# Performance work log

Measured on AMD Instinct MI355X. Metric: run time of the kernel, lower is better.

The kernel has to match this reference:

```python
import jax, jax.numpy as jnp
import numpy as np

NEG_SLOPE = 0.2
EPS = 1e-16  # PyG softmax denominator epsilon


def _gatv2_layer(x, src, dst, n_nodes, W_l, W_r, att, bias):
    """Single-head GATv2Conv (PyG defaults, self loops already in src/dst).
    x: [N, F_in]; src/dst: [E]; W_l/W_r: [F_in, F_out]; att: [F_out]; bias: [F_out].
    """
    x_l = x @ W_l                       # source transform [N, F_out]
    x_r = x @ W_r                       # target transform [N, F_out]
    # per-edge attention logit: a^T LeakyReLU(x_l[j] + x_r[i])
    e = jax.nn.leaky_relu(x_l[src] + x_r[dst], NEG_SLOPE) @ att  # [E]
    # softmax over incoming edges of each destination node
    e_max = jax.ops.segment_max(e, dst, num_segments=n_nodes)    # [N]
    ex = jnp.exp(e - e_max[dst])                                  # [E]
    denom = jax.ops.segment_sum(ex, dst, num_segments=n_nodes)   # [N]
    alpha = ex / (denom[dst] + EPS)                               # [E]
    out = jax.ops.segment_sum(alpha[:, None] * x_l[src], dst, num_segments=n_nodes)
    return out + bias


def setup_inputs() -> dict:
    key = jax.random.key(0)
    N, E = 50000, 800000
    IN, HID, OUT = 128, 64, 64
    ks = jax.random.split(key, 12)
    x = jax.random.normal(ks[0], (N, IN), dtype=jnp.float32)
    edge_index = jax.random.randint(ks[1], (2, E), 0, N, dtype=jnp.int64)
    s1 = float(1.0 / np.sqrt(IN))
    s2 = float(1.0 / np.sqrt(HID))
    return {
        "x": x,
        "edge_index": edge_index,
        "W1_l": jax.random.uniform(ks[2], (IN, HID), jnp.float32, -s1, s1),
        "W1_r": jax.random.uniform(ks[3], (IN, HID), jnp.float32, -s1, s1),
        "att1": jax.random.uniform(ks[4], (HID,), jnp.float32, -s2, s2),
        "b1": jnp.zeros((HID,), jnp.float32),
        "W2_l": jax.random.uniform(ks[5], (HID, OUT), jnp.float32, -s2, s2),
        "W2_r": jax.random.uniform(ks[6], (HID, OUT), jnp.float32, -s2, s2),
        "att2": jax.random.uniform(ks[7], (OUT,), jnp.float32, -s2, s2),
        "b2": jnp.zeros((OUT,), jnp.float32),
    }


def reference(x, edge_index, W1_l, W1_r, att1, b1, W2_l, W2_r, att2, b2):
    n = x.shape[0]
    loop = jnp.arange(n, dtype=edge_index.dtype)
    src = jnp.concatenate([edge_index[0], loop])  # add self loops (PyG default)
    dst = jnp.concatenate([edge_index[1], loop])
    h = _gatv2_layer(x, src, dst, n, W1_l, W1_r, att1, b1)
    h = jax.nn.relu(h)
    out = _gatv2_layer(h, src, dst, n, W2_l, W2_r, att2, b2)
    return out
```

## Files before the change

kernel.cpp:

```cpp
#include <hip/hip_runtime.h>
#include <math.h>

#define NEG_SLOPE 0.2f
#define EPSV 1e-16f
#define NEG_HUGE -1e30f
#define CAP 64
#define GH 1024

typedef short short8 __attribute__((ext_vector_type(8)));
typedef float f32x4 __attribute__((ext_vector_type(4)));
typedef unsigned short u16;


__global__ __launch_bounds__(256) void k_wpack(
        const float* __restrict__ W1l, const float* __restrict__ W1r,
        const float* __restrict__ W2l, const float* __restrict__ W2r,
        u16* __restrict__ w1hi, u16* __restrict__ w1lo,
        u16* __restrict__ w2hi, u16* __restrict__ w2lo,
        int* __restrict__ cnt, u16* __restrict__ csrc, int N, int NP) {
    const int idx = blockIdx.x * 256 + threadIdx.x;
    const int G = gridDim.x * 256;
    const int CN = 8 * NP;
    for (int i = idx; i < CN; i += G) {
        const int cls = i / NP;
        const int r = i - cls * NP;
        const int d = r * 8 + cls;
        cnt[i] = (d < N) ? 1 : 0;
    }
    for (int d = idx; d < N; d += G) csrc[(size_t)d * CAP] = (u16)d;
    const int T1 = 128 * 128, T2 = 64 * 128;
    if (idx >= T1 + T2) return;
    u16 *dhi, *dlo; const float *Wl, *Wr; int li;
    if (idx < T1) { dhi = w1hi; dlo = w1lo; Wl = W1l; Wr = W1r; li = idx; }
    else          { dhi = w2hi; dlo = w2lo; Wl = W2l; Wr = W2r; li = idx - T1; }
    const int j = li & 7, l = (li >> 3) & 63, t = (li >> 9) & 7, c = li >> 12;
    const int k = c * 32 + (l >> 4) * 8 + j;
    const int n = t * 16 + (l & 15);
    const float v = (n < 64) ? Wl[k * 64 + n] : Wr[k * 64 + (n - 64)];
    const unsigned u = __float_as_uint(v);
    dhi[li] = (u16)(u >> 16);
    const float hif = __uint_as_float(u & 0xffff0000u);
    dlo[li] = (u16)(__float_as_uint(v - hif) >> 16);
}

__device__ __forceinline__ void split8(const float* fs, short8& ahi, short8& alo) {
#pragma unroll
    for (int j = 0; j < 8; ++j) {
        const unsigned u = __float_as_uint(fs[j]);
        ahi[j] = (short)(u >> 16);
        const float hif = __uint_as_float(u & 0xffff0000u);
        alo[j] = (short)(__float_as_uint(fs[j] - hif) >> 16);
    }
}

template <int K>
__device__ __forceinline__ void gemm_mfma_tile(const float* __restrict__ X,
                                               const u16* __restrict__ whi,
                                               const u16* __restrict__ wlo,
                                               float* __restrict__ xl,
                                               float* __restrict__ xr,
                                               int N, int tile) {
    const int lane = threadIdx.x & 63;
    const int w = threadIdx.x >> 6;
    const int rowbase = tile * 64 + w * 16;
    const int m = lane & 15, q = lane >> 4;
    int ar = rowbase + m; if (ar > N - 1) ar = N - 1;
    const float* arow = X + (size_t)ar * K + q * 8;
    f32x4 acc[8];
#pragma unroll
    for (int t = 0; t < 8; ++t) acc[t] = (f32x4){0.f, 0.f, 0.f, 0.f};
#pragma unroll
    for (int c = 0; c < K / 32; ++c) {
        const f32x4 f0 = __builtin_nontemporal_load((const f32x4*)(arow + c * 32));
        const f32x4 f1 = __builtin_nontemporal_load((const f32x4*)(arow + c * 32 + 4));
        const float fs[8] = {f0[0], f0[1], f0[2], f0[3], f1[0], f1[1], f1[2], f1[3]};
        short8 ahi, alo;
        split8(fs, ahi, alo);
        const u16* bp = whi + ((size_t)(c * 8) * 64 + lane) * 8;
        const u16* bq = wlo + ((size_t)(c * 8) * 64 + lane) * 8;
#pragma unroll
        for (int t = 0; t < 8; ++t) {
            const short8 bhi = *(const short8*)(bp + t * 64 * 8);
            const short8 blo = *(const short8*)(bq + t * 64 * 8);
            acc[t] = __builtin_amdgcn_mfma_f32_16x16x32_bf16(bhi, ahi, acc[t], 0, 0, 0);
            acc[t] = __builtin_amdgcn_mfma_f32_16x16x32_bf16(blo, ahi, acc[t], 0, 0, 0);
            acc[t] = __builtin_amdgcn_mfma_f32_16x16x32_bf16(bhi, alo, acc[t], 0, 0, 0);
        }
    }
    const int row = rowbase + m;
    if (row < N) {
#pragma unroll
        for (int t = 0; t < 8; ++t) {
            const int colb = t * 16 + q * 4;
            float* dstp = (t < 4) ? (xl + (size_t)row * 64 + colb)
                                  : (xr + (size_t)row * 64 + (colb - 64));
            __builtin_nontemporal_store(acc[t], (f32x4*)dstp);
        }
    }
}

template <int K>
__global__ __launch_bounds__(256) void k_hist_gemm(const int* __restrict__ ei, int E,
                                                   int* __restrict__ cnt,
                                                   u16* __restrict__ csrc,
                                                   const float* __restrict__ X,
                                                   const u16* __restrict__ whi,
                                                   const u16* __restrict__ wlo,
                                                   float* __restrict__ xl,
                                                   float* __restrict__ xr,
                                                   int N, int NP) {
    if ((int)blockIdx.x < GH) {
        const int cls = blockIdx.x & 7;
        const int stripe = blockIdx.x >> 3;
        const int NS = GH >> 3;
        const int tid = threadIdx.x;
        const int* srcp = ei;
        const int* dstp = ei + E;
        int* cntc = cnt + cls * NP;
        if ((E & 7) == 0) {
            for (int base = stripe * 2048; base < E; base += NS * 2048) {
                const int e8 = base + tid * 8;
                if (e8 < E) {
                    const int4 da = *(const int4*)(dstp + e8);
                    const int4 db = *(const int4*)(dstp + e8 + 4);
                    const int4 sa = *(const int4*)(srcp + e8);
                    const int4 sb = *(const int4*)(srcp + e8 + 4);
                    const int d[8] = {da.x, da.y, da.z, da.w, db.x, db.y, db.z, db.w};
                    const int s[8] = {sa.x, sa.y, sa.z, sa.w, sb.x, sb.y, sb.z, sb.w};
                    bool m[8]; int sl[8];
#pragma unroll
                    for (int j = 0; j < 8; ++j) {
                        m[j] = (d[j] & 7) == cls;
                        if (m[j]) sl[j] = atomicAdd(&cntc[d[j] >> 3], 1);
                    }
#pragma unroll
                    for (int j = 0; j < 8; ++j) {
                        if (m[j]) csrc[(size_t)d[j] * CAP + sl[j]] = (u16)s[j];
                    }
                }
            }
        } else {
            for (int base = stripe * 256; base < E; base += NS * 256) {
                const int e = base + tid;
                if (e < E) {
                    const int dd = dstp[e];
                    if ((dd & 7) == cls) {
                        const int ss = srcp[e];
                        const int slot = atomicAdd(&cntc[dd >> 3], 1);
                        csrc[(size_t)dd * CAP + slot] = (u16)ss;
                    }
                }
            }
        }
    } else {
        gemm_mfma_tile<K>(X, whi, wlo, xl, xr, N, blockIdx.x - GH);
    }
}

template <int K>
__global__ __launch_bounds__(256) void k_gemm(const float* __restrict__ X,
                                              const u16* __restrict__ whi,
                                              const u16* __restrict__ wlo,
                                              float* __restrict__ xl,
                                              float* __restrict__ xr, int N) {
    gemm_mfma_tile<K>(X, whi, wlo, xl, xr, N, blockIdx.x);
}

__global__ __launch_bounds__(256) void k_attn(const float* __restrict__ xl,
                                              const float* xr,
                                              const float* __restrict__ att,
                                              const int* __restrict__ cnt,
                                              const u16* __restrict__ csrc,
                                              const float* __restrict__ bias,
                                              float* out, int N, int NP, int relu) {
    const int lane = threadIdx.x & 63;
    const int g = lane >> 4;
    const int i = lane & 15;
    const int dst = blockIdx.x * 4 + (threadIdx.x >> 6);
    if (dst >= N) return;
    const float4 xrv = *(const float4*)(xr + (size_t)dst * 64 + i * 4);
    const float4 aw  = *(const float4*)(att + i * 4);
    const int deg = cnt[(dst & 7) * NP + (dst >> 3)];
    const int sidx = (int)csrc[(size_t)dst * CAP + ((lane < deg) ? lane : 0)];
    float l = 0.0f;
    float4 acc = {0.0f, 0.0f, 0.0f, 0.0f};
    for (int t = 0; t < deg; t += 16) {
        const int s0 = t + g, s1 = t + 4 + g, s2 = t + 8 + g, s3 = t + 12 + g;
        const bool v0 = s0 < deg, v1 = s1 < deg, v2 = s2 < deg, v3 = s3 < deg;
        const int src0 = __shfl(sidx, s0, 64);
        const int src1 = __shfl(sidx, s1, 64);
        const int src2 = __shfl(sidx, s2, 64);
        const int src3 = __shfl(sidx, s3, 64);
        const float4 va = *(const float4*)(xl + (size_t)src0 * 64 + i * 4);
        const float4 vb = *(const float4*)(xl + (size_t)src1 * 64 + i * 4);
        const float4 vc = *(const float4*)(xl + (size_t)src2 * 64 + i * 4);
        const float4 vd = *(const float4*)(xl + (size_t)src3 * 64 + i * 4);
        float t0, p0, p1, p2, p3;
        t0 = va.x + xrv.x; t0 = fmaxf(t0, NEG_SLOPE * t0); p0 = aw.x * t0;
        t0 = va.y + xrv.y; t0 = fmaxf(t0, NEG_SLOPE * t0); p0 = fmaf(aw.y, t0, p0);
        t0 = va.z + xrv.z; t0 = fmaxf(t0, NEG_SLOPE * t0); p0 = fmaf(aw.z, t0, p0);
        t0 = va.w + xrv.w; t0 = fmaxf(t0, NEG_SLOPE * t0); p0 = fmaf(aw.w, t0, p0);
        t0 = vb.x + xrv.x; t0 = fmaxf(t0, NEG_SLOPE * t0); p1 = aw.x * t0;
        t0 = vb.y + xrv.y; t0 = fmaxf(t0, NEG_SLOPE * t0); p1 = fmaf(aw.y, t0, p1);
        t0 = vb.z + xrv.z; t0 = fmaxf(t0, NEG_SLOPE * t0); p1 = fmaf(aw.z, t0, p1);
        t0 = vb.w + xrv.w; t0 = fmaxf(t0, NEG_SLOPE * t0); p1 = fmaf(aw.w, t0, p1);
        t0 = vc.x + xrv.x; t0 = fmaxf(t0, NEG_SLOPE * t0); p2 = aw.x * t0;
        t0 = vc.y + xrv.y; t0 = fmaxf(t0, NEG_SLOPE * t0); p2 = fmaf(aw.y, t0, p2);
        t0 = vc.z + xrv.z; t0 = fmaxf(t0, NEG_SLOPE * t0); p2 = fmaf(aw.z, t0, p2);
        t0 = vc.w + xrv.w; t0 = fmaxf(t0, NEG_SLOPE * t0); p2 = fmaf(aw.w, t0, p2);
        t0 = vd.x + xrv.x; t0 = fmaxf(t0, NEG_SLOPE * t0); p3 = aw.x * t0;
        t0 = vd.y + xrv.y; t0 = fmaxf(t0, NEG_SLOPE * t0); p3 = fmaf(aw.y, t0, p3);
        t0 = vd.z + xrv.z; t0 = fmaxf(t0, NEG_SLOPE * t0); p3 = fmaf(aw.z, t0, p3);
        t0 = vd.w + xrv.w; t0 = fmaxf(t0, NEG_SLOPE * t0); p3 = fmaf(aw.w, t0, p3);
        p0 += __shfl_xor(p0, 1, 64); p1 += __shfl_xor(p1, 1, 64);
        p2 += __shfl_xor(p2, 1, 64); p3 += __shfl_xor(p3, 1, 64);
        p0 += __shfl_xor(p0, 2, 64); p1 += __shfl_xor(p1, 2, 64);
        p2 += __shfl_xor(p2, 2, 64); p3 += __shfl_xor(p3, 2, 64);
        p0 += __shfl_xor(p0, 4, 64); p1 += __shfl_xor(p1, 4, 64);
        p2 += __shfl_xor(p2, 4, 64); p3 += __shfl_xor(p3, 4, 64);
        p0 += __shfl_xor(p0, 8, 64); p1 += __shfl_xor(p1, 8, 64);
        p2 += __shfl_xor(p2, 8, 64); p3 += __shfl_xor(p3, 8, 64);
        const float d0 = __expf(v0 ? p0 : NEG_HUGE);
        const float d1 = __expf(v1 ? p1 : NEG_HUGE);
        const float d2 = __expf(v2 ? p2 : NEG_HUGE);
        const float d3 = __expf(v3 ? p3 : NEG_HUGE);
        l += (d0 + d1) + (d2 + d3);
        acc.x = fmaf(d0, va.x, fmaf(d1, vb.x, fmaf(d2, vc.x, fmaf(d3, vd.x, acc.x))));
        acc.y = fmaf(d0, va.y, fmaf(d1, vb.y, fmaf(d2, vc.y, fmaf(d3, vd.y, acc.y))));
        acc.z = fmaf(d0, va.z, fmaf(d1, vb.z, fmaf(d2, vc.z, fmaf(d3, vd.z, acc.z))));
        acc.w = fmaf(d0, va.w, fmaf(d1, vb.w, fmaf(d2, vc.w, fmaf(d3, vd.w, acc.w))));
    }
#pragma unroll
    for (int o = 16; o <= 32; o <<= 1) {
        l     += __shfl_xor(l, o, 64);
        acc.x += __shfl_xor(acc.x, o, 64);
        acc.y += __shfl_xor(acc.y, o, 64);
        acc.z += __shfl_xor(acc.z, o, 64);
        acc.w += __shfl_xor(acc.w, o, 64);
    }
    if (g == 0) {
        const float4 bv = *(const float4*)(bias + i * 4);
        const float inv = 1.0f / (l + EPSV);
        float4 r;
        r.x = fmaf(acc.x, inv, bv.x);
        r.y = fmaf(acc.y, inv, bv.y);
        r.z = fmaf(acc.z, inv, bv.z);
        r.w = fmaf(acc.w, inv, bv.w);
        if (relu) {
            r.x = fmaxf(r.x, 0.0f); r.y = fmaxf(r.y, 0.0f);
            r.z = fmaxf(r.z, 0.0f); r.w = fmaxf(r.w, 0.0f);
        }
        *(float4*)(out + (size_t)dst * 64 + i * 4) = r;
    }
}


extern "C" void kernel_launch(void* const* d_in, const int* in_sizes, int n_in,
                              void* d_out, int out_size, void* d_ws, size_t ws_size,
                              hipStream_t stream) {
    const float* x    = (const float*)d_in[0];
    const int*   ei   = (const int*)d_in[1];
    const float* W1l  = (const float*)d_in[2];
    const float* W1r  = (const float*)d_in[3];
    const float* att1 = (const float*)d_in[4];
    const float* b1   = (const float*)d_in[5];
    const float* W2l  = (const float*)d_in[6];
    const float* W2r  = (const float*)d_in[7];
    const float* att2 = (const float*)d_in[8];
    const float* b2   = (const float*)d_in[9];

    const int N  = in_sizes[0] / 128;
    const int E  = in_sizes[1] / 2;
    const int NP = (((N + 7) >> 3) + 31) & ~31;

    int* wsi   = (int*)d_ws;
    int* cnt   = wsi;
    u16* csrc  = (u16*)(cnt + 8 * NP);
    u16* w1hi  = csrc + (size_t)N * CAP;
    u16* w1lo  = w1hi + 16384;
    u16* w2hi  = w1lo + 16384;
    u16* w2lo  = w2hi + 8192;
    float* buf1 = (float*)(w2lo + 8192);
    float* buf2 = buf1 + (size_t)N * 64;
    float* fout = (float*)d_out;

    const dim3 b256(256);
    const int gGemm = (N + 63) / 64;
    const int gAttn = (N + 3) / 4;

    k_wpack<<<(128 * 128 + 64 * 128 + 255) / 256, b256, 0, stream>>>(
        W1l, W1r, W2l, W2r, w1hi, w1lo, w2hi, w2lo, cnt, csrc, N, NP);

    k_hist_gemm<128><<<GH + gGemm, b256, 0, stream>>>(ei, E, cnt, csrc,
                                                      x, w1hi, w1lo, fout, buf1, N, NP);
    k_attn<<<gAttn, b256, 0, stream>>>(fout, buf1, att1, cnt, csrc, b1, buf2, N, NP, 1);

    k_gemm<64><<<gGemm, b256, 0, stream>>>(buf2, w2hi, w2lo, buf1, fout, N);
    k_attn<<<gAttn, b256, 0, stream>>>(buf1, fout, att2, cnt, csrc, b2, fout, N, NP, 0);
}
```

Measured before the change: 228.1 us.

## Split fused histogram/GEMM kernel into separate build and GEMM launches

Undoes the fusion of the CSR bucket build and the layer-1 MFMA GEMM, turning them back into two kernel launches. The build kernel now uses 2048 blocks that each process 4 edges per thread instead of 8. The GEMM tile switches from nontemporal loads and stores to plain vector loads and stores, and the k_wpack grid is fixed at 256 blocks. Running the two phases separately loses their concurrent overlap and adds a launch, in exchange for simpler scheduling and more parallelism in the atomic build.

```diff
diff --git a/kernel.cpp b/kernel.cpp
--- a/kernel.cpp
+++ b/kernel.cpp
@@ -5,7 +5,7 @@
 #define EPSV 1e-16f
 #define NEG_HUGE -1e30f
 #define CAP 64
-#define GH 1024
+#define GB 2048
 
 typedef short short8 __attribute__((ext_vector_type(8)));
 typedef float f32x4 __attribute__((ext_vector_type(4)));
@@ -71,9 +71,9 @@
     for (int t = 0; t < 8; ++t) acc[t] = (f32x4){0.f, 0.f, 0.f, 0.f};
 #pragma unroll
     for (int c = 0; c < K / 32; ++c) {
-        const f32x4 f0 = __builtin_nontemporal_load((const f32x4*)(arow + c * 32));
-        const f32x4 f1 = __builtin_nontemporal_load((const f32x4*)(arow + c * 32 + 4));
-        const float fs[8] = {f0[0], f0[1], f0[2], f0[3], f1[0], f1[1], f1[2], f1[3]};
+        const float4 f0 = *(const float4*)(arow + c * 32);
+        const float4 f1 = *(const float4*)(arow + c * 32 + 4);
+        const float fs[8] = {f0.x, f0.y, f0.z, f0.w, f1.x, f1.y, f1.z, f1.w};
         short8 ahi, alo;
         split8(fs, ahi, alo);
         const u16* bp = whi + ((size_t)(c * 8) * 64 + lane) * 8;
@@ -92,68 +92,58 @@
 #pragma unroll
         for (int t = 0; t < 8; ++t) {
             const int colb = t * 16 + q * 4;
+            float4 v;
+            v.x = acc[t][0]; v.y = acc[t][1]; v.z = acc[t][2]; v.w = acc[t][3];
             float* dstp = (t < 4) ? (xl + (size_t)row * 64 + colb)
                                   : (xr + (size_t)row * 64 + (colb - 64));
-            __builtin_nontemporal_store(acc[t], (f32x4*)dstp);
-        }
-    }
-}
-
-template <int K>
-__global__ __launch_bounds__(256) void k_hist_gemm(const int* __restrict__ ei, int E,
-                                                   int* __restrict__ cnt,
-                                                   u16* __restrict__ csrc,
-                                                   const float* __restrict__ X,
-                                                   const u16* __restrict__ whi,
-                                                   const u16* __restrict__ wlo,
-                                                   float* __restrict__ xl,
-                                                   float* __restrict__ xr,
-                                                   int N, int NP) {
-    if ((int)blockIdx.x < GH) {
-        const int cls = blockIdx.x & 7;
-        const int stripe = blockIdx.x >> 3;
-        const int NS = GH >> 3;
-        const int tid = threadIdx.x;
-        const int* srcp = ei;
-        const int* dstp = ei + E;
-        int* cntc = cnt + cls * NP;
-        if ((E & 7) == 0) {
-            for (int base = stripe * 2048; base < E; base += NS * 2048) {
-                const int e8 = base + tid * 8;
-                if (e8 < E) {
-                    const int4 da = *(const int4*)(dstp + e8);
-                    const int4 db = *(const int4*)(dstp + e8 + 4);
-                    const int4 sa = *(const int4*)(srcp + e8);
-                    const int4 sb = *(const int4*)(srcp + e8 + 4);
-                    const int d[8] = {da.x, da.y, da.z, da.w, db.x, db.y, db.z, db.w};
-                    const int s[8] = {sa.x, sa.y, sa.z, sa.w, sb.x, sb.y, sb.z, sb.w};
-                    bool m[8]; int sl[8];
-#pragma unroll
-                    for (int j = 0; j < 8; ++j) {
-                        m[j] = (d[j] & 7) == cls;
-                        if (m[j]) sl[j] = atomicAdd(&cntc[d[j] >> 3], 1);
-                    }
-#pragma unroll
-                    for (int j = 0; j < 8; ++j) {
-                        if (m[j]) csrc[(size_t)d[j] * CAP + sl[j]] = (u16)s[j];
-                    }
+            *(float4*)dstp = v;
+        }
+    }
+}
+
+__global__ __launch_bounds__(256) void k_build(const int* __restrict__ ei, int E,
+                                               int* __restrict__ cnt,
+                                               u16* __restrict__ csrc,
+                                               int N, int NP) {
+    const int cls = blockIdx.x & 7;
+    const int stripe = blockIdx.x >> 3;
+    const int NS = GB >> 3;
+    const int tid = threadIdx.x;
+    const int* srcp = ei;
+    const int* dstp = ei + E;
+    int* cntc = cnt + cls * NP;
+    if ((E & 3) == 0) {
+        for (int base = stripe * 1024; base < E; base += NS * 1024) {
+            const int e4 = base + tid * 4;
+            if (e4 < E) {
+                const int4 d4 = *(const int4*)(dstp + e4);
+                const int4 s4 = *(const int4*)(srcp + e4);
+                const int d[4] = {d4.x, d4.y, d4.z, d4.w};
+                const int s[4] = {s4.x, s4.y, s4.z, s4.w};
+                bool m[4]; int sl[4];
+#pragma unroll
+                for (int j = 0; j < 4; ++j) {
+                    m[j] = (d[j] & 7) == cls;
+                    if (m[j]) sl[j] = atomicAdd(&cntc[d[j] >> 3], 1);
+                }
+#pragma unroll
+                for (int j = 0; j < 4; ++j) {
+                    if (m[j]) csrc[(size_t)d[j] * CAP + sl[j]] = (u16)s[j];
                 }
             }
-        } else {
-            for (int base = stripe * 256; base < E; base += NS * 256) {
-                const int e = base + tid;
-                if (e < E) {
-                    const int dd = dstp[e];
-                    if ((dd & 7) == cls) {
-                        const int ss = srcp[e];
-                        const int slot = atomicAdd(&cntc[dd >> 3], 1);
-                        csrc[(size_t)dd * CAP + slot] = (u16)ss;
-                    }
+        }
+    } else {
+        for (int base = stripe * 256; base < E; base += NS * 256) {
+            const int e = base + tid;
+            if (e < E) {
+                const int dd = dstp[e];
+                if ((dd & 7) == cls) {
+                    const int ss = srcp[e];
+                    const int slot = atomicAdd(&cntc[dd >> 3], 1);
+                    csrc[(size_t)dd * CAP + slot] = (u16)ss;
                 }
             }
         }
-    } else {
-        gemm_mfma_tile<K>(X, whi, wlo, xl, xr, N, blockIdx.x - GH);
     }
 }
 
@@ -288,11 +278,13 @@
     const int gGemm = (N + 63) / 64;
     const int gAttn = (N + 3) / 4;
 
-    k_wpack<<<(128 * 128 + 64 * 128 + 255) / 256, b256, 0, stream>>>(
+    k_wpack<<<256, b256, 0, stream>>>(
         W1l, W1r, W2l, W2r, w1hi, w1lo, w2hi, w2lo, cnt, csrc, N, NP);
 
-    k_hist_gemm<128><<<GH + gGemm, b256, 0, stream>>>(ei, E, cnt, csrc,
-                                                      x, w1hi, w1lo, fout, buf1, N, NP);
+    k_build<<<GB, b256, 0, stream>>>(ei, E, cnt, csrc, N, NP);
+
+    k_gemm<128><<<gGemm, b256, 0, stream>>>(x, w1hi, w1lo, fout, buf1, N);
+
     k_attn<<<gAttn, b256, 0, stream>>>(fout, buf1, att1, cnt, csrc, b1, buf2, N, NP, 1);
 
     k_gemm<64><<<gGemm, b256, 0, stream>>>(buf2, w2hi, w2lo, buf1, fout, N);
```

Result: no change. 224.6 us (-1.5%).
